# Performance work log

Hardware: AMD Instinct MI355X
Metric: run time of the kernel (lower is better)

The kernel has to match this reference:

```python
import jax, jax.numpy as jnp
import numpy as np

NEG = 0.01  # torch leaky_relu default slope


def conv1d(x, w, pad):
    # x: [B, C, L], w: [O, I, K], stride 1, no bias (as in FC-STGNN extractor)
    return jax.lax.conv_general_dilated(x, w, (1,), [(pad, pad)], dimension_numbers=('NCH', 'OIH', 'NCH'))


def maxpool2(x):
    # MaxPool1d(kernel=2, stride=2, padding=1); torch pads with -inf for max
    return jax.lax.reduce_window(x, -jnp.inf, jax.lax.max, (1, 1, 2), (1, 1, 2), ((0, 0), (0, 0), (1, 1)))


def pos_encoding(n, d):
    # standard sinusoidal PE table, rows 0..n-1 (n <= max_len=5000)
    pos = jnp.arange(n, dtype=jnp.float32)[:, None]
    div = jnp.exp(jnp.arange(0, d, 2, dtype=jnp.float32) * (-float(np.log(10000.0)) / d))
    pe = jnp.zeros((n, d), jnp.float32)
    pe = pe.at[:, 0::2].set(jnp.sin(pos * div))
    pe = pe.at[:, 1::2].set(jnp.cos(pos * div))
    return pe


def mpnn_block(x, gw, gb, bng, bnb, tw, tb):
    # GraphConvpoolMPNN_block_v6 with time_length=1, time_window_size=1, stride=1:
    # one window, decay mask = ones, mean-pool over the size-1 time window is identity.
    bs, two_h, N = x.shape
    X = x.reshape(bs, N, two_h)                                   # (bs*num_windows, num_node*tw, input_dim)
    h = X @ gw + gb                                               # Dot_Graph_Construction mapping
    adj = jnp.einsum('bnd,bmd->bnm', h, h)                        # dot-product adjacency
    eye = jnp.eye(N, dtype=X.dtype)
    adj = jax.nn.leaky_relu(adj - eye * 1e8, NEG)
    adj = jax.nn.softmax(adj, axis=-1) + eye
    Xb = X * bng + bnb                                            # BatchNorm1d eval (running mean 0 / var 1)
    out = jax.nn.leaky_relu(jnp.einsum('bnm,bmd->bnd', adj, Xb) @ tw + tb, NEG)  # MPNN_mk k=1
    return out                                                    # [bs, N, hidden]


def setup_inputs() -> dict:
    key = jax.random.key(0)
    ks = jax.random.split(key, 20)
    bs, D, N = 4, 128, 1024
    H, OUT, KS = 64, 32, 8        # lstmhidden_dim, lstmout_dim, conv_kernel
    HID = 64                      # hidden_dim
    TWOH = 2 * HID
    CONV_OUT = 18
    NCLS = 6
    f32 = jnp.float32
    rn = lambda k, s, sc: jax.random.normal(k, s, f32) * sc
    return {
        'x_enc': rn(ks[0], (bs, D, N), 1.0),
        'x_mark_enc': rn(ks[1], (bs, D, 4), 1.0),
        'x_dec': rn(ks[2], (bs, D // 2, N), 1.0),
        'x_mark_dec': rn(ks[3], (bs, D // 2, 4), 1.0),
        'conv_w1': rn(ks[4], (H, 1, KS), 1.0 / np.sqrt(KS)),
        'bn1_g': jnp.ones((H,), f32), 'bn1_b': jnp.zeros((H,), f32),
        'conv_w2': rn(ks[5], (2 * H, H, KS), 1.0 / np.sqrt(H * KS)),
        'bn2_g': jnp.ones((2 * H,), f32), 'bn2_b': jnp.zeros((2 * H,), f32),
        'conv_w3': rn(ks[6], (OUT, 2 * H, KS), 1.0 / np.sqrt(2 * H * KS)),
        'bn3_g': jnp.ones((OUT,), f32), 'bn3_b': jnp.zeros((OUT,), f32),
        'map2_w': rn(ks[7], (OUT * CONV_OUT, TWOH), 1.0 / np.sqrt(OUT * CONV_OUT)),
        'map2_b': jnp.zeros((TWOH,), f32),
        'map2_bn_g': jnp.ones((TWOH,), f32), 'map2_bn_b': jnp.zeros((TWOH,), f32),
        'g1_w': rn(ks[8], (TWOH, TWOH), 1.0 / np.sqrt(TWOH)), 'g1_b': jnp.zeros((TWOH,), f32),
        'm1_bn_g': jnp.ones((TWOH,), f32), 'm1_bn_b': jnp.zeros((TWOH,), f32),
        't1_w': rn(ks[9], (TWOH, HID), 1.0 / np.sqrt(TWOH)), 't1_b': jnp.zeros((HID,), f32),
        'g2_w': rn(ks[10], (TWOH, TWOH), 1.0 / np.sqrt(TWOH)), 'g2_b': jnp.zeros((TWOH,), f32),
        'm2_bn_g': jnp.ones((TWOH,), f32), 'm2_bn_b': jnp.zeros((TWOH,), f32),
        't2_w': rn(ks[11], (TWOH, HID), 1.0 / np.sqrt(TWOH)), 't2_b': jnp.zeros((HID,), f32),
        'fc1_w': rn(ks[12], (HID * 2 * N, TWOH), 1.0 / np.sqrt(HID * 2 * N)), 'fc1_b': jnp.zeros((TWOH,), f32),
        'fc2_w': rn(ks[13], (TWOH, TWOH), 1.0 / np.sqrt(TWOH)), 'fc2_b': jnp.zeros((TWOH,), f32),
        'fc3_w': rn(ks[14], (TWOH, HID), 1.0 / np.sqrt(TWOH)), 'fc3_b': jnp.zeros((HID,), f32),
        'fc4_w': rn(ks[15], (HID, NCLS), 1.0 / np.sqrt(HID)), 'fc4_b': jnp.zeros((NCLS,), f32),
    }


def reference(x_enc, x_mark_enc, x_dec, x_mark_dec,
              conv_w1, bn1_g, bn1_b, conv_w2, bn2_g, bn2_b, conv_w3, bn3_g, bn3_b,
              map2_w, map2_b, map2_bn_g, map2_bn_b,
              g1_w, g1_b, m1_bn_g, m1_bn_b, t1_w, t1_b,
              g2_w, g2_b, m2_bn_g, m2_bn_b, t2_w, t2_b,
              fc1_w, fc1_b, fc2_w, fc2_b, fc3_w, fc3_b, fc4_w, fc4_b):
    bs, D, N = x_enc.shape
    k = conv_w1.shape[-1]
    # nonlin_map: 1D-CNN feature extractor over each (sample, node) signal
    a = jnp.swapaxes(x_enc.reshape(bs * N, D, 1), 1, 2)           # [bs*N, 1, D]
    a = maxpool2(jax.nn.relu(conv1d(a, conv_w1, k // 2) * bn1_g[None, :, None] + bn1_b[None, :, None]))
    a = maxpool2(jax.nn.relu(conv1d(a, conv_w2, 4) * bn2_g[None, :, None] + bn2_b[None, :, None]))
    a = maxpool2(jax.nn.relu(conv1d(a, conv_w3, 4) * bn3_g[None, :, None] + bn3_b[None, :, None]))
    a = a.reshape(bs * N, -1)                                     # [bs*N, lstmout_dim*conv_out]
    # nonlin_map2: Linear + BatchNorm1d (eval mode affine)
    a = (a @ map2_w + map2_b) * map2_bn_g + map2_bn_b             # [bs*N, 2h]
    two_h = a.shape[-1]
    # positional encoding with the exact reshape/transpose traffic of the torch forward
    x = jnp.swapaxes(a.reshape(bs, N, two_h), 1, 2).reshape(bs * N, two_h)
    x = x + pos_encoding(bs * N, two_h)
    x = jnp.swapaxes(x.reshape(bs, N, two_h), 1, 2)               # [bs, 2h, N]
    # two graph MPNN branches
    o1 = mpnn_block(x, g1_w, g1_b, m1_bn_g, m1_bn_b, t1_w, t1_b)
    o2 = mpnn_block(x, g2_w, g2_b, m2_bn_g, m2_bn_b, t2_w, t2_b)
    f = jnp.concatenate([o1.reshape(bs, -1), o2.reshape(bs, -1)], axis=-1)
    # MLP head
    f = jax.nn.relu(f @ fc1_w + fc1_b)
    f = jax.nn.relu(f @ fc2_w + fc2_b)
    f = jax.nn.relu(f @ fc3_w + fc3_b)
    return f @ fc4_w + fc4_b                                      # [bs, n_class]
```

## Files before the change

### kernel.cpp

```cpp
#include <hip/hip_runtime.h>
#include <math.h>

#define NEG 0.01f
__device__ __forceinline__ float lrelu(float v){ return v > 0.f ? v : NEG*v; }
__device__ __forceinline__ float frelu(float v){ return v > 0.f ? v : 0.f; }

typedef __attribute__((ext_vector_type(8))) short bf16x8;
typedef __attribute__((ext_vector_type(4))) float f32x4;

__device__ __forceinline__ unsigned short f2bf(float x){
    unsigned int u = __float_as_uint(x);
    unsigned int r = (u + 0x7FFFu + ((u>>16)&1u)) >> 16;
    return (unsigned short)r;
}
__device__ __forceinline__ float bf2f(unsigned short h){
    return __uint_as_float(((unsigned int)h) << 16);
}

__global__ __launch_bounds__(256) void k_prep(const float* __restrict__ w2, const float* __restrict__ w3,
    const float* __restrict__ m2w,
    unsigned short* __restrict__ w2s, unsigned short* __restrict__ w3s, unsigned short* __restrict__ m2wbT)
{
    int gid = blockIdx.x*256 + threadIdx.x;
    if (gid < 73728) {
        int j = gid / 576, f = gid % 576;
        m2wbT[gid] = f2bf(m2w[f*128 + j]);
    }
    if (gid < 65536) {
        int jj = gid & 7, q = (gid>>3)&3, o = (gid>>5)&127, ks = (gid>>12)&1, k = gid>>13;
        int c = ks*32 + q*8 + jj;
        w2s[gid] = f2bf(w2[o*512 + c*8 + k]);
    }
    if (gid < 32768) {
        int jj = gid & 7, q = (gid>>3)&3, o = (gid>>5)&31, ks = (gid>>10)&3, k = gid>>12;
        int c = ks*32 + q*8 + jj;
        w3s[gid] = f2bf(w3[o*1024 + c*8 + k]);
    }
}

__global__ __launch_bounds__(256) void k_conv(
    const float* __restrict__ xenc,
    const float* __restrict__ w1, const float* __restrict__ g1, const float* __restrict__ b1,
    const unsigned short* __restrict__ w2s, const float* __restrict__ g2, const float* __restrict__ b2,
    const unsigned short* __restrict__ w3s, const float* __restrict__ g3, const float* __restrict__ b3,
    unsigned short* __restrict__ aflatG)
{
    __shared__ __align__(16) unsigned char smraw[38464];
    float* sigp = (float*)smraw;
    unsigned short* p1T = (unsigned short*)(smraw + 576);
    unsigned short* p2T = (unsigned short*)(smraw + 10304);
    unsigned short* c2o = (unsigned short*)(smraw + 21056);
    float* c3o = (float*)(smraw + 21056);

    const int t = threadIdx.x;
    const int s = blockIdx.x;

    {
        unsigned int* zz = (unsigned int*)(smraw + 576);
        for (int i = t; i < 5120; i += 256) zz[i] = 0u;
        if (t < 144) sigp[t] = 0.f;
    }
    __syncthreads();
    if (t < 128) sigp[4 + t] = xenc[(size_t)s*128 + t];
    __syncthreads();

    {
        const int c = t & 63, qg = t >> 6;
        float wr[8];
        #pragma unroll
        for (int k = 0; k < 8; ++k) wr[k] = w1[c*8 + k];
        const float g = g1[c], b = b1[c];
        const int qs = qg*17;
        float win[9];
        {
            int base = 2*qs - 1;
            #pragma unroll
            for (int x = 0; x < 9; ++x) win[x] = (base + x >= 0) ? sigp[base + x] : 0.f;
        }
        #pragma unroll
        for (int j = 0; j < 17; ++j) {
            int q = qs + j;
            float s0 = 0.f, s1 = 0.f;
            #pragma unroll
            for (int k = 0; k < 8; ++k) { s0 += win[k]*wr[k]; s1 += win[k+1]*wr[k]; }
            float v = frelu(s1*g + b);
            if (q > 0) v = fmaxf(v, frelu(s0*g + b));
            if (q < 65) {
                int row = q + 4;
                p1T[row*64 + (((c>>3) ^ (row&7))<<3) + (c&7)] = f2bf(v);
            }
            #pragma unroll
            for (int x = 0; x < 7; ++x) win[x] = win[x+2];
            win[7] = sigp[2*q + 8];
            win[8] = sigp[2*q + 9];
        }
    }
    __syncthreads();

    {
        const int wv = t >> 6, l = t & 63, lg = l >> 4, lr = l & 15;
        f32x4 acc[2][5] = {};
        for (int k = 0; k < 8; ++k) {
            for (int ks = 0; ks < 2; ++ks) {
                bf16x8 af[2];
                #pragma unroll
                for (int oi = 0; oi < 2; ++oi) {
                    int o = (wv*2 + oi)*16 + lr;
                    af[oi] = *(const bf16x8*)(w2s + ((((k*2 + ks)*128 + o)*4 + lg)<<3));
                }
                #pragma unroll
                for (int nt = 0; nt < 5; ++nt) {
                    int row = nt*16 + lr + k; row = row > 75 ? 75 : row;
                    int q = ks*4 + lg;
                    bf16x8 bfv = *(const bf16x8*)(p1T + row*64 + ((q ^ (row&7))<<3));
                    acc[0][nt] = __builtin_amdgcn_mfma_f32_16x16x32_bf16(af[0], bfv, acc[0][nt], 0,0,0);
                    acc[1][nt] = __builtin_amdgcn_mfma_f32_16x16x32_bf16(af[1], bfv, acc[1][nt], 0,0,0);
                }
            }
        }
        #pragma unroll
        for (int oi = 0; oi < 2; ++oi)
            #pragma unroll
            for (int nt = 0; nt < 5; ++nt)
                #pragma unroll
                for (int r = 0; r < 4; ++r) {
                    int o = (wv*2 + oi)*16 + lg*4 + r;
                    int p = nt*16 + lr;
                    if (p < 66) c2o[o*68 + p] = f2bf(frelu(acc[oi][nt][r] * g2[o] + b2[o]));
                }
    }
    __syncthreads();

    for (int idx = t; idx < 4352; idx += 256) {
        int o = idx & 127, q = idx >> 7;
        unsigned short v = (q <= 32) ? c2o[o*68 + 2*q] : (unsigned short)0;
        if (q > 0) { unsigned short v2 = c2o[o*68 + 2*q - 1]; v = (v2 > v) ? v2 : v; }
        int row = q + 4;
        p2T[row*128 + (((o>>3) ^ (row&15))<<3) + (o&7)] = v;
    }
    __syncthreads();

    {
        const int wv = t >> 6, l = t & 63, lg = l >> 4, lr = l & 15;
        const int ot = wv & 1, ntb = (wv >> 1) * 2;
        const int ncnt = (wv < 2) ? 2 : 1;
        f32x4 acc[2] = {};
        for (int k = 0; k < 8; ++k) {
            for (int ks = 0; ks < 4; ++ks) {
                int o = ot*16 + lr;
                bf16x8 af = *(const bf16x8*)(w3s + ((((k*4 + ks)*32 + o)*4 + lg)<<3));
                int q = ks*4 + lg;
                #pragma unroll
                for (int ni = 0; ni < 2; ++ni) {
                    if (ni < ncnt) {
                        int row = (ntb + ni)*16 + lr + k; row = row > 41 ? 41 : row;
                        bf16x8 bfv = *(const bf16x8*)(p2T + row*128 + ((q ^ (row&15))<<3));
                        acc[ni] = __builtin_amdgcn_mfma_f32_16x16x32_bf16(af, bfv, acc[ni], 0,0,0);
                    }
                }
            }
        }
        #pragma unroll
        for (int ni = 0; ni < 2; ++ni) if (ni < ncnt)
            #pragma unroll
            for (int r = 0; r < 4; ++r) {
                int o = ot*16 + lg*4 + r;
                int p = (ntb + ni)*16 + lr;
                if (p < 35) c3o[o*36 + p] = frelu(acc[ni][r] * g3[o] + b3[o]);
            }
    }
    __syncthreads();

    for (int idx = t; idx < 576; idx += 256) {
        int o = idx / 18, q = idx % 18;
        float v = c3o[o*36 + 2*q];
        if (q > 0) v = fmaxf(v, c3o[o*36 + 2*q - 1]);
        aflatG[(size_t)s*576 + idx] = f2bf(v);
    }
}

__global__ __launch_bounds__(256) void k_map2(const unsigned short* __restrict__ aflatG,
    const unsigned short* __restrict__ m2wbT,
    const float* __restrict__ m2b, const float* __restrict__ m2g, const float* __restrict__ m2bb,
    float* __restrict__ a2)
{
    const int t = threadIdx.x, wv = t>>6, l = t&63, lg = l>>4, lr = l&15;
    const int s0 = blockIdx.x*64;
    f32x4 acc[8] = {};
    for (int ks = 0; ks < 18; ++ks) {
        bf16x8 a = *(const bf16x8*)(aflatG + (size_t)(s0 + wv*16 + lr)*576 + ks*32 + lg*8);
        #pragma unroll
        for (int nt = 0; nt < 8; ++nt) {
            bf16x8 b = *(const bf16x8*)(m2wbT + (size_t)(nt*16 + lr)*576 + ks*32 + lg*8);
            acc[nt] = __builtin_amdgcn_mfma_f32_16x16x32_bf16(a, b, acc[nt], 0,0,0);
        }
    }
    #pragma unroll
    for (int nt = 0; nt < 8; ++nt)
        #pragma unroll
        for (int r = 0; r < 4; ++r) {
            int s2 = s0 + wv*16 + lg*4 + r;
            int j = nt*16 + lr;
            a2[(size_t)s2*128 + j] = (acc[nt][r] + m2b[j]) * m2g[j] + m2bb[j];
        }
}

__global__ __launch_bounds__(256) void k_buildx(const float* __restrict__ a2, float* __restrict__ X)
{
    __shared__ double dvt[64];
    const int t = threadIdx.x;
    if (t < 64) dvt[t] = exp((double)(2*t) * (-9.210340371976184/128.0));
    __syncthreads();
    int e = blockIdx.x*256 + t;
    int b = e >> 17;
    int r = e & 131071;
    int i = r >> 7, d = r & 127;
    int row = b*1024 + (d & 7)*128 + (i >> 3);
    int col = (i & 7)*16 + (d >> 3);
    float v = a2[row*128 + col];
    int per = b*1024 + (i & 7)*128 + d;
    int pc  = i >> 3;
    double ang = (double)per * dvt[pc >> 1];
    const double TWO_PI = 6.283185307179586476925287;
    double kk = floor(ang * (1.0/TWO_PI) + 0.5);
    float red = (float)(ang - kk * TWO_PI);
    float pe = (pc & 1) ? __cosf(red) : __sinf(red);
    X[e] = v + pe;
}

__global__ __launch_bounds__(256) void k_hmat(const float* __restrict__ X,
    const float* __restrict__ g1w, const float* __restrict__ g1b,
    const float* __restrict__ g2w, const float* __restrict__ g2b,
    unsigned short* __restrict__ Hbhi1, unsigned short* __restrict__ Hblo1,
    unsigned short* __restrict__ Hbhi2, unsigned short* __restrict__ Hblo2)
{
    const int br = blockIdx.y;
    const float* gw = br ? g2w : g1w;
    const float* gb = br ? g2b : g1b;
    unsigned short* Hh = br ? Hbhi2 : Hbhi1;
    unsigned short* Hl = br ? Hblo2 : Hblo1;
    int e = blockIdx.x*256 + threadIdx.x;
    int srow = e >> 7, j = e & 127;
    const float* xr = X + (size_t)srow*128;
    float acc = gb[j];
    for (int k = 0; k < 128; ++k) acc += xr[k] * gw[k*128 + j];
    unsigned short hh = f2bf(acc);
    Hh[e] = hh;
    Hl[e] = f2bf(acc - bf2f(hh));
}

__global__ __launch_bounds__(256) void k_scores(
    const unsigned short* __restrict__ Hbhi, const unsigned short* __restrict__ Hblo,
    float* __restrict__ S)
{
    __shared__ __align__(16) unsigned short HiH[64*64];
    __shared__ __align__(16) unsigned short HiL[64*64];
    __shared__ __align__(16) unsigned short HjH[64*64];
    __shared__ __align__(16) unsigned short HjL[64*64];
    const int b = blockIdx.z;
    const int i0 = blockIdx.y * 64, j0 = blockIdx.x * 64;
    const int t = threadIdx.x;
    const int w = t >> 6, l = t & 63, lr = l & 15, h = l >> 4;
    const size_t hb = (size_t)b * 1024 * 128;

    f32x4 acc[4] = {};
    for (int kh = 0; kh < 2; ++kh) {
        __syncthreads();
        #pragma unroll
        for (int it = 0; it < 4; ++it) {
            int g = it*256 + t;
            int mat = g >> 9;
            int gg = g & 511;
            int row = gg >> 3, ch = gg & 7;
            int base0 = mat ? j0 : i0;
            size_t src = hb + (size_t)(base0 + row)*128 + kh*64 + ch*8;
            uint4 vh = *(const uint4*)(Hbhi + src);
            uint4 vl = *(const uint4*)(Hblo + src);
            int sw = ch ^ (row & 7);
            unsigned short* dh = (mat ? HjH : HiH) + row*64 + sw*8;
            unsigned short* dl = (mat ? HjL : HiL) + row*64 + sw*8;
            *(uint4*)dh = vh;
            *(uint4*)dl = vl;
        }
        __syncthreads();
        #pragma unroll
        for (int kc = 0; kc < 2; ++kc) {
            int swA = (((kc*4 + h) ^ (lr & 7)) << 3);
            bf16x8 ah = *(const bf16x8*)&HiH[(w*16 + lr)*64 + swA];
            bf16x8 al = *(const bf16x8*)&HiL[(w*16 + lr)*64 + swA];
            #pragma unroll
            for (int jt = 0; jt < 4; ++jt) {
                bf16x8 bh = *(const bf16x8*)&HjH[(jt*16 + lr)*64 + swA];
                bf16x8 bl = *(const bf16x8*)&HjL[(jt*16 + lr)*64 + swA];
                acc[jt] = __builtin_amdgcn_mfma_f32_16x16x32_bf16(ah, bh, acc[jt], 0,0,0);
                acc[jt] = __builtin_amdgcn_mfma_f32_16x16x32_bf16(ah, bl, acc[jt], 0,0,0);
                acc[jt] = __builtin_amdgcn_mfma_f32_16x16x32_bf16(al, bh, acc[jt], 0,0,0);
            }
        }
    }
    float* Sb = S + (size_t)b*1024*1024;
    #pragma unroll
    for (int jt = 0; jt < 4; ++jt) {
        #pragma unroll
        for (int r = 0; r < 4; ++r) {
            int i = i0 + w*16 + h*4 + r;
            int j = j0 + jt*16 + lr;
            float x = acc[jt][r];
            if (i == j) x -= 1e8f;
            Sb[(size_t)i*1024 + j] = lrelu(x);
        }
    }
}

__global__ __launch_bounds__(256) void k_rowstat(const float* __restrict__ S,
                                                 float* __restrict__ mrow, float* __restrict__ linv)
{
    __shared__ float red[256];
    const int b = blockIdx.y, i = blockIdx.x, t = threadIdx.x;
    const float* row = S + (size_t)b*1024*1024 + (size_t)i*1024;
    float4 v = *(const float4*)&row[t*4];
    float mx = fmaxf(fmaxf(v.x,v.y), fmaxf(v.z,v.w));
    red[t] = mx; __syncthreads();
    for (int s2 = 128; s2 > 0; s2 >>= 1) { if (t < s2) red[t] = fmaxf(red[t], red[t+s2]); __syncthreads(); }
    mx = red[0]; __syncthreads();
    float e = (__expf(v.x-mx) + __expf(v.y-mx)) + (__expf(v.z-mx) + __expf(v.w-mx));
    red[t] = e; __syncthreads();
    for (int s2 = 128; s2 > 0; s2 >>= 1) { if (t < s2) red[t] += red[t+s2]; __syncthreads(); }
    if (t == 0) { mrow[b*1024 + i] = mx; linv[b*1024 + i] = 1.f / red[0]; }
}

__global__ __launch_bounds__(256) void k_xbbt(const float* __restrict__ X,
    const float* __restrict__ bng1, const float* __restrict__ bnb1,
    const float* __restrict__ bng2, const float* __restrict__ bnb2,
    unsigned short* __restrict__ XbbThi, unsigned short* __restrict__ XbbTlo)
{
    __shared__ float Xl[64][132];
    const int t = threadIdx.x;
    const int j0 = blockIdx.x*64, b = blockIdx.y, br = blockIdx.z;
    {
        int r2 = t >> 2, dseg = (t & 3)*32;
        const float* src = X + ((size_t)(b*1024 + j0 + r2))*128 + dseg;
        #pragma unroll
        for (int q = 0; q < 8; ++q) {
            float4 v = *(const float4*)(src + q*4);
            Xl[r2][dseg + q*4 + 0] = v.x;
            Xl[r2][dseg + q*4 + 1] = v.y;
            Xl[r2][dseg + q*4 + 2] = v.z;
            Xl[r2][dseg + q*4 + 3] = v.w;
        }
    }
    __syncthreads();
    const int d = t >> 1, seg = t & 1;
    const float g  = (br ? bng2 : bng1)[d];
    const float bb = (br ? bnb2 : bnb1)[d];
    unsigned short* dsth = XbbThi + (size_t)br*524288 + ((size_t)(b*128 + d))*1024 + j0 + seg*32;
    unsigned short* dstl = XbbTlo + (size_t)br*524288 + ((size_t)(b*128 + d))*1024 + j0 + seg*32;
    #pragma unroll
    for (int g8 = 0; g8 < 4; ++g8) {
        unsigned int hu[4], lu[4];
        #pragma unroll
        for (int q = 0; q < 4; ++q) {
            float v0 = Xl[seg*32 + g8*8 + 2*q    ][d]*g + bb;
            float v1 = Xl[seg*32 + g8*8 + 2*q + 1][d]*g + bb;
            unsigned short h0 = f2bf(v0), h1 = f2bf(v1);
            hu[q] = (unsigned int)h0 | ((unsigned int)h1 << 16);
            lu[q] = (unsigned int)f2bf(v0 - bf2f(h0)) | ((unsigned int)f2bf(v1 - bf2f(h1)) << 16);
        }
        *(uint4*)(dsth + g8*8) = make_uint4(hu[0],hu[1],hu[2],hu[3]);
        *(uint4*)(dstl + g8*8) = make_uint4(lu[0],lu[1],lu[2],lu[3]);
    }
}

__global__ __launch_bounds__(256) void k_pvmm(
    const float* __restrict__ S1, const float* __restrict__ S2, const float* __restrict__ X,
    const float* __restrict__ bng1, const float* __restrict__ bnb1,
    const float* __restrict__ bng2, const float* __restrict__ bnb2,
    const float* __restrict__ mrow, const float* __restrict__ linv,
    const unsigned short* __restrict__ XbbThi, const unsigned short* __restrict__ XbbTlo,
    float* __restrict__ P)
{
    __shared__ __align__(16) unsigned short ElH[16*64];
    __shared__ __align__(16) unsigned short ElL[16*64];
    const int t = threadIdx.x;
    const int w = t >> 6, l = t & 63, lr = l & 15, h = l >> 4;
    const int i0 = blockIdx.x * 16;
    const int b = blockIdx.y;
    const int br = blockIdx.z;
    const float* S = br ? S2 : S1;
    const float* bng = br ? bng2 : bng1;
    const float* bnb = br ? bnb2 : bnb1;
    const float* mr = mrow + br*4096 + b*1024;
    const float* lv = linv + br*4096 + b*1024;
    const unsigned short* Bh = XbbThi + (size_t)br*524288 + (size_t)b*131072;
    const unsigned short* Bl = XbbTlo + (size_t)br*524288 + (size_t)b*131072;

    const int srow = t >> 4, jseg = t & 15;
    const float mi = mr[i0 + srow];
    const int j0s = jseg*4;
    const int eoff = srow*64 + (((j0s>>3) ^ (srow&7))<<3) + (j0s&7);

    f32x4 acc[2] = {};
    for (int ch = 0; ch < 16; ++ch) {
        const int jb = ch*64;
        __syncthreads();
        {
            float4 sv = *(const float4*)(S + ((size_t)(b*1024 + i0 + srow))*1024 + jb + j0s);
            float e0 = __expf(sv.x - mi), e1 = __expf(sv.y - mi);
            float e2 = __expf(sv.z - mi), e3 = __expf(sv.w - mi);
            unsigned short h0 = f2bf(e0), h1 = f2bf(e1), h2 = f2bf(e2), h3 = f2bf(e3);
            uint2 vh, vl;
            vh.x = (unsigned int)h0 | ((unsigned int)h1 << 16);
            vh.y = (unsigned int)h2 | ((unsigned int)h3 << 16);
            vl.x = (unsigned int)f2bf(e0 - bf2f(h0)) | ((unsigned int)f2bf(e1 - bf2f(h1)) << 16);
            vl.y = (unsigned int)f2bf(e2 - bf2f(h2)) | ((unsigned int)f2bf(e3 - bf2f(h3)) << 16);
            *(uint2*)(ElH + eoff) = vh;
            *(uint2*)(ElL + eoff) = vl;
        }
        __syncthreads();
        #pragma unroll
        for (int kc = 0; kc < 2; ++kc) {
            int swA = (((kc*4 + h) ^ (lr & 7)) << 3);
            bf16x8 ah = *(const bf16x8*)&ElH[lr*64 + swA];
            bf16x8 al = *(const bf16x8*)&ElL[lr*64 + swA];
            #pragma unroll
            for (int n2 = 0; n2 < 2; ++n2) {
                int nt = w*2 + n2;
                size_t boff = (size_t)(nt*16 + lr)*1024 + jb + kc*32 + h*8;
                bf16x8 bh = *(const bf16x8*)(Bh + boff);
                bf16x8 bl = *(const bf16x8*)(Bl + boff);
                acc[n2] = __builtin_amdgcn_mfma_f32_16x16x32_bf16(ah, bh, acc[n2], 0,0,0);
                acc[n2] = __builtin_amdgcn_mfma_f32_16x16x32_bf16(ah, bl, acc[n2], 0,0,0);
                acc[n2] = __builtin_amdgcn_mfma_f32_16x16x32_bf16(al, bh, acc[n2], 0,0,0);
            }
        }
    }
    #pragma unroll
    for (int r = 0; r < 4; ++r) {
        int i = i0 + h*4 + r;
        float inv = lv[i];
        #pragma unroll
        for (int n2 = 0; n2 < 2; ++n2) {
            int d = (w*2 + n2)*16 + lr;
            float xv = X[((size_t)(b*1024 + i))*128 + d] * bng[d] + bnb[d];
            P[((size_t)(br*4096 + b*1024 + i))*128 + d] = acc[n2][r]*inv + xv;
        }
    }
}

__global__ __launch_bounds__(256) void k_pv(const float* __restrict__ S, const float* __restrict__ X,
                                            const float* __restrict__ bng, const float* __restrict__ bnb,
                                            const float* __restrict__ mrowG, const float* __restrict__ linvG,
                                            float* __restrict__ P)
{
    __shared__ __align__(16) float Sl[16*65];
    __shared__ __align__(16) float Xl[64*132];
    const int b = blockIdx.y, i0 = blockIdx.x*16, t = threadIdx.x;
    const int il = t >> 4, dg = t & 15;
    const int sj = t & 63, sil = t >> 6;
    const int xd = t & 127, xj = t >> 7;
    const float bg = bng[xd], bb = bnb[xd];
    float mr[4];
    #pragma unroll
    for (int m2 = 0; m2 < 4; ++m2) mr[m2] = mrowG[b*1024 + i0 + sil*4 + m2];
    float acc[8] = {};
    const float* Sb = S + (size_t)b*1024*1024;
    const float* Xb = X + (size_t)b*1024*128;
    for (int c = 0; c < 16; ++c) {
        int jb = c*64;
        __syncthreads();
        #pragma unroll
        for (int m2 = 0; m2 < 4; ++m2) {
            int r2 = sil*4 + m2;
            Sl[r2*65 + sj] = __expf(Sb[(size_t)(i0+r2)*1024 + jb + sj] - mr[m2]);
        }
        #pragma unroll
        for (int m2 = 0; m2 < 32; ++m2) {
            int jc = xj + 2*m2;
            Xl[jc*132 + xd] = Xb[(size_t)(jb+jc)*128 + xd] * bg + bb;
        }
        __syncthreads();
        for (int jc = 0; jc < 64; ++jc) {
            float sv = Sl[il*65 + jc];
            float4 x0 = *(const float4*)&Xl[jc*132 + dg*8];
            float4 x1 = *(const float4*)&Xl[jc*132 + dg*8 + 4];
            acc[0] += sv*x0.x; acc[1] += sv*x0.y; acc[2] += sv*x0.z; acc[3] += sv*x0.w;
            acc[4] += sv*x1.x; acc[5] += sv*x1.y; acc[6] += sv*x1.z; acc[7] += sv*x1.w;
        }
    }
    int i = i0 + il;
    float inv = linvG[b*1024 + i];
    const float* xr = Xb + (size_t)i*128 + dg*8;
    float* pr = P + (size_t)(b*1024 + i)*128 + dg*8;
    #pragma unroll
    for (int z = 0; z < 8; ++z) {
        float xv = xr[z] * bng[dg*8+z] + bnb[dg*8+z];
        pr[z] = acc[z]*inv + xv;
    }
}

__global__ __launch_bounds__(256) void k_tproj(const float* __restrict__ P, const float* __restrict__ tw,
                                               const float* __restrict__ tb, float* __restrict__ O)
{
    int idx = blockIdx.x*256 + threadIdx.x;
    int srow = idx >> 6, e = idx & 63;
    const float* pr = P + (size_t)srow*128;
    float acc = tb[e];
    for (int d = 0; d < 128; ++d) acc += pr[d] * tw[d*64 + e];
    O[idx] = lrelu(acc);
}

__global__ __launch_bounds__(256) void k_tproj2(const float* __restrict__ P,
    const float* __restrict__ t1w, const float* __restrict__ t1b,
    const float* __restrict__ t2w, const float* __restrict__ t2b,
    float* __restrict__ O)
{
    int idx = blockIdx.x*256 + threadIdx.x;
    int srow = idx >> 6, e = idx & 63;
    int br = srow >> 12;
    const float* tw = br ? t2w : t1w;
    const float* tb = br ? t2b : t1b;
    const float* pr = P + (size_t)srow*128;
    float acc = tb[e];
    for (int d = 0; d < 128; ++d) acc += pr[d] * tw[d*64 + e];
    O[idx] = lrelu(acc);
}

__global__ __launch_bounds__(256) void k_fc1(const float* __restrict__ O1, const float* __restrict__ O2,
                                             const float* __restrict__ w, float* __restrict__ pbuf)
{
    __shared__ float red[4*512];
    const int t = threadIdx.x;
    const int wv = t >> 6, l = t & 63;
    const int gwid = blockIdx.x*4 + wv;
    float acc[4][2] = {};
    int base = gwid*64;
    for (int tt = 0; tt < 64; ++tt) {
        int row = base + tt;
        float2 wvv = *(const float2*)&w[(size_t)row*128 + l*2];
        #pragma unroll
        for (int b = 0; b < 4; ++b) {
            float fb = (row < 65536) ? O1[b*65536 + row] : O2[b*65536 + row - 65536];
            acc[b][0] += fb * wvv.x;
            acc[b][1] += fb * wvv.y;
        }
    }
    #pragma unroll
    for (int b = 0; b < 4; ++b) {
        red[wv*512 + b*128 + l*2]   = acc[b][0];
        red[wv*512 + b*128 + l*2+1] = acc[b][1];
    }
    __syncthreads();
    for (int rep = 0; rep < 2; ++rep) {
        int col = rep*256 + t;
        pbuf[(size_t)blockIdx.x*512 + col] = red[col] + red[512+col] + red[1024+col] + red[1536+col];
    }
}

__global__ __launch_bounds__(256) void k_red(const float* __restrict__ pbuf, float* __restrict__ pbuf2)
{
    int col = blockIdx.x*8 + (threadIdx.x >> 5);
    int lane = threadIdx.x & 31;
    float acc = 0.f;
    for (int it = 0; it < 16; ++it)
        acc += pbuf[(size_t)(lane + it*32)*512 + col];
    #pragma unroll
    for (int s2 = 16; s2 >= 1; s2 >>= 1) acc += __shfl_xor(acc, s2, 32);
    if (lane == 0) pbuf2[col] = acc;
}

__global__ __launch_bounds__(256) void k_head2(const float* __restrict__ pbuf2,
    const float* __restrict__ fc1b, const float* __restrict__ fc2w, const float* __restrict__ fc2b,
    const float* __restrict__ fc3w, const float* __restrict__ fc3b,
    const float* __restrict__ fc4w, const float* __restrict__ fc4b,
    float* __restrict__ out)
{
    __shared__ float r1[512], r2[512], r3[256];
    const int t = threadIdx.x;
    for (int rep = 0; rep < 2; ++rep) {
        int idx = rep*256 + t;
        r1[idx] = frelu(pbuf2[idx] + fc1b[idx & 127]);
    }
    __syncthreads();
    for (int rep = 0; rep < 2; ++rep) {
        int idx = rep*256 + t;
        int b = idx >> 7, j = idx & 127;
        float acc = fc2b[j];
        for (int k = 0; k < 128; ++k) acc += r1[b*128+k]*fc2w[k*128+j];
        r2[idx] = frelu(acc);
    }
    __syncthreads();
    {
        int b = t >> 6, e2 = t & 63;
        float acc = fc3b[e2];
        for (int k = 0; k < 128; ++k) acc += r2[b*128+k]*fc3w[k*64+e2];
        r3[t] = frelu(acc);
    }
    __syncthreads();
    if (t < 24) {
        int b = t/6, c = t%6;
        float acc = fc4b[c];
        for (int k = 0; k < 64; ++k) acc += r3[b*64+k]*fc4w[k*6+c];
        out[b*6+c] = acc;
    }
}

extern "C" void kernel_launch(void* const* d_in, const int* in_sizes, int n_in,
                              void* d_out, int out_size, void* d_ws, size_t ws_size,
                              hipStream_t stream)
{
    (void)in_sizes; (void)n_in; (void)out_size;
    const float* xenc = (const float*)d_in[0];
    const float* w1   = (const float*)d_in[4];
    const float* g1   = (const float*)d_in[5];
    const float* b1   = (const float*)d_in[6];
    const float* w2   = (const float*)d_in[7];
    const float* g2   = (const float*)d_in[8];
    const float* b2   = (const float*)d_in[9];
    const float* w3   = (const float*)d_in[10];
    const float* g3   = (const float*)d_in[11];
    const float* b3   = (const float*)d_in[12];
    const float* m2w  = (const float*)d_in[13];
    const float* m2b  = (const float*)d_in[14];
    const float* m2g  = (const float*)d_in[15];
    const float* m2bb = (const float*)d_in[16];
    const float* g1w  = (const float*)d_in[17];
    const float* g1b  = (const float*)d_in[18];
    const float* m1g  = (const float*)d_in[19];
    const float* m1b  = (const float*)d_in[20];
    const float* t1w  = (const float*)d_in[21];
    const float* t1b  = (const float*)d_in[22];
    const float* g2w  = (const float*)d_in[23];
    const float* g2bv = (const float*)d_in[24];
    const float* mm2g = (const float*)d_in[25];
    const float* mm2b = (const float*)d_in[26];
    const float* t2w  = (const float*)d_in[27];
    const float* t2b  = (const float*)d_in[28];
    const float* fc1w = (const float*)d_in[29];
    const float* fc1b = (const float*)d_in[30];
    const float* fc2w = (const float*)d_in[31];
    const float* fc2b = (const float*)d_in[32];
    const float* fc3w = (const float*)d_in[33];
    const float* fc3b = (const float*)d_in[34];
    const float* fc4w = (const float*)d_in[35];
    const float* fc4b = (const float*)d_in[36];

    char* ws = (char*)d_ws;
    float* a2   = (float*)(ws);
    float* X    = (float*)(ws + (2u<<20));
    unsigned short* Hbhi1 = (unsigned short*)(ws + (4u<<20));
    unsigned short* Hblo1 = (unsigned short*)(ws + (5u<<20));
    unsigned short* Hbhi2 = (unsigned short*)(ws);
    unsigned short* Hblo2 = (unsigned short*)(ws + (1u<<20));
    float* S1   = (float*)(ws + (6u<<20));
    unsigned short* aflatG = (unsigned short*)(ws + (6u<<20));
    unsigned short* w2s    = (unsigned short*)(ws + (6u<<20) + 5242880);
    unsigned short* w3s    = (unsigned short*)(ws + (6u<<20) + 5242880 + 131072);
    unsigned short* m2wbT  = (unsigned short*)(ws + (6u<<20) + 5242880 + 196608);
    float* pbuf2 = (float*)(ws + (6u<<20));

    k_prep<<<288, 256, 0, stream>>>(w2, w3, m2w, w2s, w3s, m2wbT);
    k_conv<<<4096, 256, 0, stream>>>(xenc, w1,g1,b1, w2s,g2,b2, w3s,g3,b3, aflatG);
    k_map2<<<64, 256, 0, stream>>>(aflatG, m2wbT, m2b, m2g, m2bb, a2);
    k_buildx<<<2048, 256, 0, stream>>>(a2, X);
    k_hmat<<<dim3(2048,2), 256, 0, stream>>>(X, g1w, g1b, g2w, g2bv,
                                             Hbhi1, Hblo1, Hbhi2, Hblo2);

    if (ws_size >= ((size_t)49 << 20)) {
        float* S2   = (float*)(ws + (22u<<20));
        float* P    = (float*)(ws + (38u<<20));
        float* O    = (float*)(ws + (42u<<20));
        float* pbuf = (float*)(ws + (44u<<20));
        float* mrow = (float*)(ws + (44u<<20));
        float* linv = (float*)(ws + (44u<<20) + 65536);
        unsigned short* XbbThi = (unsigned short*)(ws + (45u<<20));
        unsigned short* XbbTlo = (unsigned short*)(ws + (47u<<20));
        float* O1 = O;
        float* O2 = O + 262144;

        k_xbbt<<<dim3(16,4,2), 256, 0, stream>>>(X, m1g, m1b, mm2g, mm2b, XbbThi, XbbTlo);
        k_scores <<<dim3(16,16,4), 256, 0, stream>>>(Hbhi1, Hblo1, S1);
        k_scores <<<dim3(16,16,4), 256, 0, stream>>>(Hbhi2, Hblo2, S2);
        k_rowstat<<<dim3(1024,4), 256, 0, stream>>>(S1, mrow, linv);
        k_rowstat<<<dim3(1024,4), 256, 0, stream>>>(S2, mrow + 4096, linv + 4096);
        k_pvmm<<<dim3(64,4,2), 256, 0, stream>>>(S1, S2, X, m1g, m1b, mm2g, mm2b,
                                                 mrow, linv, XbbThi, XbbTlo, P);
        k_tproj2<<<2048, 256, 0, stream>>>(P, t1w, t1b, t2w, t2b, O);
        k_fc1 <<<512, 256, 0, stream>>>(O1, O2, fc1w, pbuf);
        k_red <<<64, 256, 0, stream>>>(pbuf, pbuf2);
        k_head2<<<1, 256, 0, stream>>>(pbuf2, fc1b, fc2w, fc2b, fc3w, fc3b, fc4w, fc4b, (float*)d_out);
    } else {
        float* P    = (float*)(ws + (22u<<20));
        float* O1   = (float*)(ws + (24u<<20));
        float* O2   = (float*)(ws + (25u<<20));
        float* pbuf = (float*)(ws + (26u<<20));
        float* mrow = (float*)(ws + (26u<<20));
        float* linv = (float*)(ws + (26u<<20) + 65536);

        k_scores <<<dim3(16,16,4), 256, 0, stream>>>(Hbhi1, Hblo1, S1);
        k_rowstat<<<dim3(1024,4), 256, 0, stream>>>(S1, mrow, linv);
        k_pv     <<<dim3(64,4), 256, 0, stream>>>(S1, X, m1g, m1b, mrow, linv, P);
        k_tproj  <<<1024, 256, 0, stream>>>(P, t1w, t1b, O1);
        k_scores <<<dim3(16,16,4), 256, 0, stream>>>(Hbhi2, Hblo2, S1);
        k_rowstat<<<dim3(1024,4), 256, 0, stream>>>(S1, mrow, linv);
        k_pv     <<<dim3(64,4), 256, 0, stream>>>(S1, X, mm2g, mm2b, mrow, linv, P);
        k_tproj  <<<1024, 256, 0, stream>>>(P, t2w, t2b, O2);
        k_fc1 <<<512, 256, 0, stream>>>(O1, O2, fc1w, pbuf);
        k_red <<<64, 256, 0, stream>>>(pbuf, pbuf2);
        k_head2<<<1, 256, 0, stream>>>(pbuf2, fc1b, fc2w, fc2b, fc3w, fc3b, fc4w, fc4b, (float*)d_out);
    }
}
```

Baseline: 288.8 us.

## Fuse maxpool into conv2/conv3 MFMA epilogues via permuted columns and lane shuffles

Permutes the output positions assigned to MFMA lanes so that adjacent pool pairs sit 8 lanes apart. The pooling max is then done with a __shfl_xor in registers and written straight into the next stage's swizzled LDS layout. This removes the c2o/c3o staging buffers, two LDS round-trips and one barrier per block, and shrinks shared memory so more blocks can fit per CU. BN scale and shift loads are hoisted, and bf16 conversion moves to the HIP intrinsic, which may round differently at edge cases.

Measured after the change: 279.0 us. 3.4% less time.

```diff
diff --git a/kernel.cpp b/kernel.cpp
--- a/kernel.cpp
+++ b/kernel.cpp
@@ -1,4 +1,5 @@
 #include <hip/hip_runtime.h>
+#include <hip/hip_bf16.h>
 #include <math.h>
 
 #define NEG 0.01f
@@ -15,6 +16,10 @@
 }
 __device__ __forceinline__ float bf2f(unsigned short h){
     return __uint_as_float(((unsigned int)h) << 16);
+}
+__device__ __forceinline__ unsigned short F2B(float x){
+    __hip_bfloat16 h = __float2bfloat16(x);
+    return *reinterpret_cast<unsigned short*>(&h);
 }
 
 __global__ __launch_bounds__(256) void k_prep(const float* __restrict__ w2, const float* __restrict__ w3,
@@ -45,12 +50,11 @@
     const unsigned short* __restrict__ w3s, const float* __restrict__ g3, const float* __restrict__ b3,
     unsigned short* __restrict__ aflatG)
 {
-    __shared__ __align__(16) unsigned char smraw[38464];
+    __shared__ __align__(16) unsigned char smraw[22208];
     float* sigp = (float*)smraw;
     unsigned short* p1T = (unsigned short*)(smraw + 576);
     unsigned short* p2T = (unsigned short*)(smraw + 10304);
-    unsigned short* c2o = (unsigned short*)(smraw + 21056);
-    float* c3o = (float*)(smraw + 21056);
+    unsigned short* astage = (unsigned short*)(smraw + 21056);
 
     const int t = threadIdx.x;
     const int s = blockIdx.x;
@@ -87,7 +91,7 @@
             if (q > 0) v = fmaxf(v, frelu(s0*g + b));
             if (q < 65) {
                 int row = q + 4;
-                p1T[row*64 + (((c>>3) ^ (row&7))<<3) + (c&7)] = f2bf(v);
+                p1T[row*64 + (((c>>3) ^ (row&7))<<3) + (c&7)] = F2B(v);
             }
             #pragma unroll
             for (int x = 0; x < 7; ++x) win[x] = win[x+2];
@@ -99,6 +103,7 @@
 
     {
         const int wv = t >> 6, l = t & 63, lg = l >> 4, lr = l & 15;
+        const int pbase = ((lr & 7) << 1) + (lr >> 3) - 1;
         f32x4 acc[2][5] = {};
         for (int k = 0; k < 8; ++k) {
             for (int ks = 0; ks < 2; ++ks) {
@@ -108,35 +113,49 @@
                     int o = (wv*2 + oi)*16 + lr;
                     af[oi] = *(const bf16x8*)(w2s + ((((k*2 + ks)*128 + o)*4 + lg)<<3));
                 }
+                const int q = ks*4 + lg;
                 #pragma unroll
                 for (int nt = 0; nt < 5; ++nt) {
-                    int row = nt*16 + lr + k; row = row > 75 ? 75 : row;
-                    int q = ks*4 + lg;
+                    int row = nt*16 + pbase + k; row = row > 75 ? 75 : row;
                     bf16x8 bfv = *(const bf16x8*)(p1T + row*64 + ((q ^ (row&7))<<3));
                     acc[0][nt] = __builtin_amdgcn_mfma_f32_16x16x32_bf16(af[0], bfv, acc[0][nt], 0,0,0);
                     acc[1][nt] = __builtin_amdgcn_mfma_f32_16x16x32_bf16(af[1], bfv, acc[1][nt], 0,0,0);
                 }
             }
         }
+        float ga[2][4], ba[2][4];
         #pragma unroll
         for (int oi = 0; oi < 2; ++oi)
             #pragma unroll
-            for (int nt = 0; nt < 5; ++nt)
+            for (int r = 0; r < 4; ++r) {
+                int o = (wv*2 + oi)*16 + lg*4 + r;
+                ga[oi][r] = g2[o]; ba[oi][r] = b2[o];
+            }
+        #pragma unroll
+        for (int oi = 0; oi < 2; ++oi)
+            #pragma unroll
+            for (int nt = 0; nt < 5; ++nt) {
+                int p = nt*16 + pbase;
+                bool valid = (p >= 0) && (p <= 65);
+                float vv[4];
                 #pragma unroll
                 for (int r = 0; r < 4; ++r) {
-                    int o = (wv*2 + oi)*16 + lg*4 + r;
-                    int p = nt*16 + lr;
-                    if (p < 66) c2o[o*68 + p] = f2bf(frelu(acc[oi][nt][r] * g2[o] + b2[o]));
+                    float v = frelu(acc[oi][nt][r]*ga[oi][r] + ba[oi][r]);
+                    vv[r] = valid ? v : -3.0e38f;
                 }
-    }
-    __syncthreads();
-
-    for (int idx = t; idx < 4352; idx += 256) {
-        int o = idx & 127, q = idx >> 7;
-        unsigned short v = (q <= 32) ? c2o[o*68 + 2*q] : (unsigned short)0;
-        if (q > 0) { unsigned short v2 = c2o[o*68 + 2*q - 1]; v = (v2 > v) ? v2 : v; }
-        int row = q + 4;
-        p2T[row*128 + (((o>>3) ^ (row&15))<<3) + (o&7)] = v;
+                float pv[4];
+                #pragma unroll
+                for (int r = 0; r < 4; ++r) pv[r] = fmaxf(vv[r], __shfl_xor(vv[r], 8));
+                int q = nt*8 + (lr & 7);
+                if ((lr >> 3) == 0 && q < 34) {
+                    int row2 = q + 4;
+                    int o0 = (wv*2 + oi)*16 + lg*4;
+                    uint2 pk;
+                    pk.x = (unsigned int)F2B(pv[0]) | ((unsigned int)F2B(pv[1]) << 16);
+                    pk.y = (unsigned int)F2B(pv[2]) | ((unsigned int)F2B(pv[3]) << 16);
+                    *(uint2*)&p2T[row2*128 + (((o0>>3) ^ (row2&15))<<3) + (o0&7)] = pk;
+                }
+            }
     }
     __syncthreads();
 
@@ -144,39 +163,54 @@
         const int wv = t >> 6, l = t & 63, lg = l >> 4, lr = l & 15;
         const int ot = wv & 1, ntb = (wv >> 1) * 2;
         const int ncnt = (wv < 2) ? 2 : 1;
+        const int pbase = ((lr & 7) << 1) + (lr >> 3) - 1;
         f32x4 acc[2] = {};
         for (int k = 0; k < 8; ++k) {
             for (int ks = 0; ks < 4; ++ks) {
                 int o = ot*16 + lr;
                 bf16x8 af = *(const bf16x8*)(w3s + ((((k*4 + ks)*32 + o)*4 + lg)<<3));
-                int q = ks*4 + lg;
+                const int q = ks*4 + lg;
                 #pragma unroll
                 for (int ni = 0; ni < 2; ++ni) {
                     if (ni < ncnt) {
-                        int row = (ntb + ni)*16 + lr + k; row = row > 41 ? 41 : row;
+                        int row = (ntb + ni)*16 + pbase + k; row = row > 41 ? 41 : row;
                         bf16x8 bfv = *(const bf16x8*)(p2T + row*128 + ((q ^ (row&15))<<3));
                         acc[ni] = __builtin_amdgcn_mfma_f32_16x16x32_bf16(af, bfv, acc[ni], 0,0,0);
                     }
                 }
             }
         }
-        #pragma unroll
-        for (int ni = 0; ni < 2; ++ni) if (ni < ncnt)
+        float g3v[4], b3v[4];
+        #pragma unroll
+        for (int r = 0; r < 4; ++r) {
+            int o = ot*16 + lg*4 + r;
+            g3v[r] = g3[o]; b3v[r] = b3[o];
+        }
+        #pragma unroll
+        for (int ni = 0; ni < 2; ++ni) if (ni < ncnt) {
+            int p = (ntb + ni)*16 + pbase;
+            bool valid = (p >= 0) && (p <= 34);
+            float vv[4];
             #pragma unroll
             for (int r = 0; r < 4; ++r) {
-                int o = ot*16 + lg*4 + r;
-                int p = (ntb + ni)*16 + lr;
-                if (p < 35) c3o[o*36 + p] = frelu(acc[ni][r] * g3[o] + b3[o]);
-            }
-    }
-    __syncthreads();
-
-    for (int idx = t; idx < 576; idx += 256) {
-        int o = idx / 18, q = idx % 18;
-        float v = c3o[o*36 + 2*q];
-        if (q > 0) v = fmaxf(v, c3o[o*36 + 2*q - 1]);
-        aflatG[(size_t)s*576 + idx] = f2bf(v);
-    }
+                float v = frelu(acc[ni][r]*g3v[r] + b3v[r]);
+                vv[r] = valid ? v : -3.0e38f;
+            }
+            float pv[4];
+            #pragma unroll
+            for (int r = 0; r < 4; ++r) pv[r] = fmaxf(vv[r], __shfl_xor(vv[r], 8));
+            int q = (ntb + ni)*8 + (lr & 7);
+            if ((lr >> 3) == 0 && q < 18) {
+                #pragma unroll
+                for (int r = 0; r < 4; ++r)
+                    astage[(ot*16 + lg*4 + r)*18 + q] = F2B(pv[r]);
+            }
+        }
+    }
+    __syncthreads();
+
+    for (int idx = t; idx < 576; idx += 256)
+        aflatG[(size_t)s*576 + idx] = astage[idx];
 }
 
 __global__ __launch_bounds__(256) void k_map2(const unsigned short* __restrict__ aflatG,
```
